# Performance work log

Measured on AMD Instinct MI355X. Metric: run time of the kernel, lower is better.

The kernel has to match this reference:

```python
import math
import jax, jax.numpy as jnp
import numpy as np

IN_CH = 512
KEY = 512
VAL = 512
B, T = 8, 2048
SQRT_KEY = math.sqrt(float(KEY))


def setup_inputs() -> dict:
    key = jax.random.key(0)
    ks = jax.random.split(key, 7)
    s_in = 1.0 / math.sqrt(IN_CH)
    return {
        "x": jax.random.normal(ks[0], (B, T, IN_CH), dtype=jnp.float32),
        "Wq": jax.random.uniform(ks[1], (IN_CH, KEY), jnp.float32, -s_in, s_in),
        "bq": jax.random.uniform(ks[2], (KEY,), jnp.float32, -s_in, s_in),
        "Wk": jax.random.uniform(ks[3], (IN_CH, KEY), jnp.float32, -s_in, s_in),
        "bk": jax.random.uniform(ks[4], (KEY,), jnp.float32, -s_in, s_in),
        "Wv": jax.random.uniform(ks[5], (IN_CH, VAL), jnp.float32, -s_in, s_in),
        "bv": jax.random.uniform(ks[6], (VAL,), jnp.float32, -s_in, s_in),
    }


def reference(x, Wq, bq, Wk, bk, Wv, bv):
    # x: [B, T, C]
    q = x @ Wq + bq          # [B, T, K]
    k = x @ Wk + bk          # [B, T, K]
    v = x @ Wv + bv          # [B, T, V]
    logits = jnp.einsum("btk,bsk->bts", q, k)  # [B, T(q), T(kv)]
    mask = jnp.tril(jnp.ones((T, T), dtype=bool))  # causal: key s <= query t
    logits = jnp.where(mask[None, :, :], logits, -jnp.inf)
    # NOTE: original torch code softmaxes over dim=1 (the QUERY axis) — kept faithful.
    probs = jax.nn.softmax(logits / SQRT_KEY, axis=1)
    read = jnp.einsum("bts,bsv->btv", probs, v)  # [B, T, V]
    return jnp.concatenate((x, read), axis=2)    # [B, T, C+V]
```

## Files before the change

### kernel.cpp

```cpp
#include <hip/hip_runtime.h>
#include <hip/hip_bf16.h>
#include <math.h>

#define BATCH 8
#define SEQ   2048
#define CH    512
#define ROWS  (BATCH * SEQ)
#define INVSQ 0.044194173824159216f

#define BM 128
#define BK 32
#define TILE_ELEMS (BM * BK)
#define TP 68

typedef __attribute__((ext_vector_type(8))) __bf16 bf16x8;
typedef __attribute__((ext_vector_type(4))) float f32x4;

__device__ inline unsigned short f2bf(float f) {
    unsigned u = __builtin_bit_cast(unsigned, f);
    u += 0x7fffu + ((u >> 16) & 1u);
    return (unsigned short)(u >> 16);
}
__device__ inline float bf2f(unsigned short s) {
    unsigned u = ((unsigned)s) << 16;
    return __builtin_bit_cast(float, u);
}

__device__ __forceinline__ void stage_tile(
    const unsigned short* __restrict__ gbase, size_t stride,
    unsigned short* lds, int wave, int lane)
{
#pragma unroll
    for (int j = 0; j < 2; ++j) {
        int chunk = wave * 2 + j;
        int row = chunk * 16 + (lane >> 2);
        const unsigned short* g = gbase + (size_t)row * stride + ((lane & 3) << 3);
        __builtin_amdgcn_global_load_lds(
            (const __attribute__((address_space(1))) unsigned int*)g,
            (__attribute__((address_space(3))) unsigned int*)(lds + (chunk << 9)),
            16, 0, 0);
    }
}

__device__ __forceinline__ void load_frags(
    const unsigned short* lds, int w0, int l16, int quad, bf16x8* f)
{
#pragma unroll
    for (int r = 0; r < 4; ++r)
        f[r] = *(const bf16x8*)(lds + (w0 + r * 16 + l16) * BK + quad * 8);
}

__global__ __launch_bounds__(256) void fuse_x_kernel(
    const float* __restrict__ x, unsigned short* __restrict__ xb,
    float* __restrict__ out, float* __restrict__ Z)
{
    if (blockIdx.x < 64) Z[blockIdx.x * 256 + threadIdx.x] = 0.f;
    size_t base = ((size_t)blockIdx.x * 256 + threadIdx.x) * 8;
    size_t row = base >> 9, c = base & 511;
    float4 v0 = *(const float4*)(x + base);
    float4 v1 = *(const float4*)(x + base + 4);
    float* o = out + row * 1024 + c;
    *(float4*)o = v0;
    *(float4*)(o + 4) = v1;
    alignas(16) unsigned short t[8];
    t[0] = f2bf(v0.x); t[1] = f2bf(v0.y); t[2] = f2bf(v0.z); t[3] = f2bf(v0.w);
    t[4] = f2bf(v1.x); t[5] = f2bf(v1.y); t[6] = f2bf(v1.z); t[7] = f2bf(v1.w);
    *(uint4*)(xb + base) = *(const uint4*)t;
}

__global__ __launch_bounds__(256) void transpose_w_kernel(
    const float* __restrict__ Wq, const float* __restrict__ Wk,
    const float* __restrict__ Wv, unsigned short* __restrict__ Wt)
{
    __shared__ unsigned short T[64 * TP];
    const int k0 = blockIdx.x * 64, n0 = blockIdx.y * 64, w = blockIdx.z;
    const float* W = (w == 0) ? Wq : (w == 1) ? Wk : Wv;
    const int tid = threadIdx.x;
#pragma unroll
    for (int i = 0; i < 2; ++i) {
        int slot = tid + i * 256;
        int kr = slot >> 3, c8 = (slot & 7) << 3;
        float4 a = *(const float4*)(W + (size_t)(k0 + kr) * CH + n0 + c8);
        float4 b = *(const float4*)(W + (size_t)(k0 + kr) * CH + n0 + c8 + 4);
        T[(c8 + 0) * TP + kr] = f2bf(a.x); T[(c8 + 1) * TP + kr] = f2bf(a.y);
        T[(c8 + 2) * TP + kr] = f2bf(a.z); T[(c8 + 3) * TP + kr] = f2bf(a.w);
        T[(c8 + 4) * TP + kr] = f2bf(b.x); T[(c8 + 5) * TP + kr] = f2bf(b.y);
        T[(c8 + 6) * TP + kr] = f2bf(b.z); T[(c8 + 7) * TP + kr] = f2bf(b.w);
    }
    __syncthreads();
#pragma unroll
    for (int i = 0; i < 2; ++i) {
        int slot = tid + i * 256;
        int nr = slot >> 3, k8 = (slot & 7) << 3;
        uint2 lo = *(const uint2*)(T + nr * TP + k8);
        uint2 hi = *(const uint2*)(T + nr * TP + k8 + 4);
        uint4 u; u.x = lo.x; u.y = lo.y; u.z = hi.x; u.w = hi.y;
        *(uint4*)(Wt + ((size_t)w * CH + n0 + nr) * CH + k0 + k8) = u;
    }
}

__global__ __launch_bounds__(256) void transpose_v_kernel(
    const unsigned short* __restrict__ vb, const float* __restrict__ Z,
    unsigned short* __restrict__ Vt)
{
    __shared__ unsigned short T[64 * TP];
    const int s0 = blockIdx.x * 64, v0 = blockIdx.y * 64, b = blockIdx.z;
    const int tid = threadIdx.x;
#pragma unroll
    for (int i = 0; i < 2; ++i) {
        int slot = tid + i * 256;
        int sr = slot >> 3, c8 = (slot & 7) << 3;
        float inv = 1.0f / Z[b * SEQ + s0 + sr];
        uint4 raw = *(const uint4*)(vb + ((size_t)b * SEQ + s0 + sr) * CH + v0 + c8);
        const unsigned short* p = (const unsigned short*)&raw;
#pragma unroll
        for (int j = 0; j < 8; ++j)
            T[(c8 + j) * TP + sr] = f2bf(bf2f(p[j]) * inv);
    }
    __syncthreads();
#pragma unroll
    for (int i = 0; i < 2; ++i) {
        int slot = tid + i * 256;
        int vr = slot >> 3, s8 = (slot & 7) << 3;
        uint2 lo = *(const uint2*)(T + vr * TP + s8);
        uint2 hi = *(const uint2*)(T + vr * TP + s8 + 4);
        uint4 u; u.x = lo.x; u.y = lo.y; u.z = hi.x; u.w = hi.y;
        *(uint4*)(Vt + ((size_t)b * CH + v0 + vr) * SEQ + s0 + s8) = u;
    }
}

#define MFMA_ROW(r, af) \
    acc[r][0] = __builtin_amdgcn_mfma_f32_16x16x32_bf16(af, b0, acc[r][0], 0, 0, 0); \
    acc[r][1] = __builtin_amdgcn_mfma_f32_16x16x32_bf16(af, b1, acc[r][1], 0, 0, 0); \
    acc[r][2] = __builtin_amdgcn_mfma_f32_16x16x32_bf16(af, b2, acc[r][2], 0, 0, 0); \
    acc[r][3] = __builtin_amdgcn_mfma_f32_16x16x32_bf16(af, b3, acc[r][3], 0, 0, 0);

#define PIPELINE_LOOP                                                         \
    stageA(0); stageB(0); stageB(1);                                          \
    asm volatile("s_waitcnt vmcnt(2)" ::: "memory");                          \
    __builtin_amdgcn_s_barrier();                                             \
    __builtin_amdgcn_sched_barrier(0);                                        \
    _Pragma("unroll")                                                         \
    for (int U = 0; U < 16; ++U) {                                            \
        const unsigned short* Ab = lds + (U & 1) * 4096;                      \
        const unsigned short* Bb = lds + 8192 + (U & 1) * 8192;               \
        bf16x8 a0, a1, b0, b1, b2, b3;                                        \
        b0 = *(const bf16x8*)(Bb + (brow +  0) * 32 + rswz);                  \
        b1 = *(const bf16x8*)(Bb + (brow + 16) * 32 + rswz);                  \
        b2 = *(const bf16x8*)(Bb + (brow + 32) * 32 + rswz);                  \
        b3 = *(const bf16x8*)(Bb + (brow + 48) * 32 + rswz);                  \
        a0 = *(const bf16x8*)(Ab + (arow +  0) * 32 + rswz);                  \
        a1 = *(const bf16x8*)(Ab + (arow + 16) * 32 + rswz);                  \
        stageA(U + 1);                                                        \
        __builtin_amdgcn_s_barrier();                                         \
        asm volatile("s_waitcnt lgkmcnt(0)" ::: "memory");                    \
        __builtin_amdgcn_sched_barrier(0);                                    \
        __builtin_amdgcn_s_setprio(1);                                        \
        MFMA_ROW(0, a0);                                                      \
        MFMA_ROW(1, a1);                                                      \
        __builtin_amdgcn_s_setprio(0);                                        \
        __builtin_amdgcn_s_barrier();                                         \
        __builtin_amdgcn_sched_barrier(0);                                    \
        a0 = *(const bf16x8*)(Ab + (arow + 32) * 32 + rswz);                  \
        a1 = *(const bf16x8*)(Ab + (arow + 48) * 32 + rswz);                  \
        stageB(U + 2);                                                        \
        __builtin_amdgcn_s_barrier();                                         \
        asm volatile("s_waitcnt lgkmcnt(0)" ::: "memory");                    \
        __builtin_amdgcn_sched_barrier(0);                                    \
        __builtin_amdgcn_s_setprio(1);                                        \
        MFMA_ROW(2, a0);                                                      \
        MFMA_ROW(3, a1);                                                      \
        __builtin_amdgcn_s_setprio(0);                                        \
        if (U <= 13)      asm volatile("s_waitcnt vmcnt(2)" ::: "memory");    \
        else if (U == 14) asm volatile("s_waitcnt vmcnt(0)" ::: "memory");    \
        __builtin_amdgcn_s_barrier();                                         \
        __builtin_amdgcn_sched_barrier(0);                                    \
    }

__global__ __launch_bounds__(512, 2) void qkv8_kernel(
    const unsigned short* __restrict__ xb, const unsigned short* __restrict__ Wt,
    const float* __restrict__ bq, const float* __restrict__ bk,
    const float* __restrict__ bv, unsigned short* __restrict__ qkv)
{
    __shared__ unsigned short lds[24576];
    const int tid = threadIdx.x;
    const int lane = tid & 63, wave = tid >> 6;
    const int waveA = wave >> 2;
    const int waveB = wave & 3;
    const int quad = lane >> 4, l16 = lane & 15;

    int id = (int)blockIdx.x;
    id = (id & 7) * 96 + (id >> 3);
    const int xt = id / 12, wt = id - xt * 12;
    const int xrow0 = xt << 8, wrow0 = wt << 7;

    const unsigned short* __restrict__ Wg = Wt + (size_t)wrow0 * CH;
    const unsigned short* __restrict__ Xg = xb + (size_t)xrow0 * CH;

    const int srow = tid >> 2;
    const int scol = (((tid & 3) ^ ((tid >> 3) & 3)) << 3);
    const size_t ga  = (size_t)srow * CH + scol;
    const size_t gb1 = (size_t)(srow + 128) * CH + scol;
    const int wdst = wave * 512;
    const int rswz = ((quad ^ ((l16 >> 1) & 3)) << 3);
    const int arow = waveA * 64 + l16;
    const int brow = waveB * 64 + l16;

    f32x4 acc[4][4] = {};

    auto stageA = [&](int V) {
        if (V >= 16) return;
        const unsigned short* g = Wg + ga + V * 32;
        unsigned short* d = lds + (V & 1) * 4096 + wdst;
        __builtin_amdgcn_global_load_lds(
            (const __attribute__((address_space(1))) unsigned int*)g,
            (__attribute__((address_space(3))) unsigned int*)d, 16, 0, 0);
    };
    auto stageB = [&](int V) {
        if (V >= 16) return;
        const unsigned short* g0 = Xg + ga + V * 32;
        const unsigned short* g1 = Xg + gb1 + V * 32;
        unsigned short* d = lds + 8192 + (V & 1) * 8192 + wdst;
        __builtin_amdgcn_global_load_lds(
            (const __attribute__((address_space(1))) unsigned int*)g0,
            (__attribute__((address_space(3))) unsigned int*)d, 16, 0, 0);
        __builtin_amdgcn_global_load_lds(
            (const __attribute__((address_space(1))) unsigned int*)g1,
            (__attribute__((address_space(3))) unsigned int*)(d + 4096), 16, 0, 0);
    };

    PIPELINE_LOOP

    const int which = wrow0 >> 9;
    const float* bias = (which == 0) ? bq : (which == 1) ? bk : bv;
    const float scale = (which == 0) ? INVSQ : 1.0f;
    unsigned short* outw = qkv + (size_t)which * ROWS * CH;
    const int colblk = wrow0 & 511;
#pragma unroll
    for (int r = 0; r < 4; ++r) {
        int colb = colblk + waveA * 64 + r * 16 + quad * 4;
        float4 b4 = *(const float4*)(bias + colb);
#pragma unroll
        for (int c = 0; c < 4; ++c) {
            int m = xrow0 + waveB * 64 + c * 16 + l16;
            alignas(8) unsigned short pk[4];
            pk[0] = f2bf((acc[r][c][0] + b4.x) * scale);
            pk[1] = f2bf((acc[r][c][1] + b4.y) * scale);
            pk[2] = f2bf((acc[r][c][2] + b4.z) * scale);
            pk[3] = f2bf((acc[r][c][3] + b4.w) * scale);
            *(uint2*)(outw + (size_t)m * CH + colb) = *(const uint2*)pk;
        }
    }
}

__global__ __launch_bounds__(512, 2) void logits8_kernel(
    const unsigned short* __restrict__ qb, const unsigned short* __restrict__ kb,
    unsigned short* __restrict__ E, float* __restrict__ Z)
{
    __shared__ unsigned short lds[24576];
    const int tid = threadIdx.x;
    const int lane = tid & 63, wave = tid >> 6;
    const int waveA = wave >> 2;
    const int waveB = wave & 3;
    const int quad = lane >> 4, l16 = lane & 15;

    const int b = (int)blockIdx.x & 7;
    const int i = (int)blockIdx.x >> 3;
    int tt2 = (int)((sqrtf(4.f * (float)i + 1.f) - 1.f) * 0.5f);
    int st = i - tt2 * (tt2 + 1);
    while (st < 0)           { --tt2; st = i - tt2 * (tt2 + 1); }
    while (st > 2 * tt2 + 1) { ++tt2; st = i - tt2 * (tt2 + 1); }
    const int m0s = st << 7;
    const int n0t = tt2 << 8;

    const unsigned short* __restrict__ Wg = kb + ((size_t)b * SEQ + m0s) * CH;
    const unsigned short* __restrict__ Xg = qb + ((size_t)b * SEQ + n0t) * CH;

    const int srow = tid >> 2;
    const int scol = (((tid & 3) ^ ((tid >> 3) & 3)) << 3);
    const size_t ga  = (size_t)srow * CH + scol;
    const size_t gb1 = (size_t)(srow + 128) * CH + scol;
    const int wdst = wave * 512;
    const int rswz = ((quad ^ ((l16 >> 1) & 3)) << 3);
    const int arow = waveA * 64 + l16;
    const int brow = waveB * 64 + l16;

    f32x4 acc[4][4] = {};

    auto stageA = [&](int V) {
        if (V >= 16) return;
        const unsigned short* g = Wg + ga + V * 32;
        unsigned short* d = lds + (V & 1) * 4096 + wdst;
        __builtin_amdgcn_global_load_lds(
            (const __attribute__((address_space(1))) unsigned int*)g,
            (__attribute__((address_space(3))) unsigned int*)d, 16, 0, 0);
    };
    auto stageB = [&](int V) {
        if (V >= 16) return;
        const unsigned short* g0 = Xg + ga + V * 32;
        const unsigned short* g1 = Xg + gb1 + V * 32;
        unsigned short* d = lds + 8192 + (V & 1) * 8192 + wdst;
        __builtin_amdgcn_global_load_lds(
            (const __attribute__((address_space(1))) unsigned int*)g0,
            (__attribute__((address_space(3))) unsigned int*)d, 16, 0, 0);
        __builtin_amdgcn_global_load_lds(
            (const __attribute__((address_space(1))) unsigned int*)g1,
            (__attribute__((address_space(3))) unsigned int*)(d + 4096), 16, 0, 0);
    };

    PIPELINE_LOOP

#pragma unroll
    for (int r = 0; r < 4; ++r) {
        int sb = m0s + waveA * 64 + r * 16 + quad * 4;
        float ev[4][4];
#pragma unroll
        for (int c = 0; c < 4; ++c) {
            int t = n0t + waveB * 64 + c * 16 + l16;
#pragma unroll
            for (int reg = 0; reg < 4; ++reg)
                ev[c][reg] = (sb + reg <= t) ? __expf(acc[r][c][reg]) : 0.f;
        }
#pragma unroll
        for (int reg = 0; reg < 4; ++reg) {
            float z = ev[0][reg] + ev[1][reg] + ev[2][reg] + ev[3][reg];
            z += __shfl_xor(z, 1);
            z += __shfl_xor(z, 2);
            z += __shfl_xor(z, 4);
            z += __shfl_xor(z, 8);
            if (l16 == 0) atomicAdd(&Z[b * SEQ + sb + reg], z);
        }
#pragma unroll
        for (int c = 0; c < 4; ++c) {
            int t = n0t + waveB * 64 + c * 16 + l16;
            alignas(8) unsigned short pk[4];
            pk[0] = f2bf(ev[c][0]); pk[1] = f2bf(ev[c][1]);
            pk[2] = f2bf(ev[c][2]); pk[3] = f2bf(ev[c][3]);
            *(uint2*)(E + ((size_t)b * SEQ + t) * SEQ + sb) = *(const uint2*)pk;
        }
    }
}
#undef PIPELINE_LOOP
#undef MFMA_ROW

__global__ __launch_bounds__(256) void read_kernel(
    const unsigned short* __restrict__ E, const unsigned short* __restrict__ Vt,
    float* __restrict__ out)
{
    __shared__ unsigned short As[2 * TILE_ELEMS];
    __shared__ unsigned short Bs[2 * TILE_ELEMS];
    const int id = blockIdx.x;
    const int b = id & 7;
    const int rem = id >> 3;
    const int mv = rem & 3;
    const int r0 = rem >> 2;
    const int tt = (r0 < 8) ? r0 : 23 - r0;
    const int m0v = mv * BM;
    const int n0t = tt * BM;
    const int Kmax = (tt + 1) * BM;
    const int tid = threadIdx.x;
    const int lane = tid & 63, wave = tid >> 6;
    const int wm = (wave >> 1) * 64, wn = (wave & 1) * 64;
    const int quad = lane >> 4, l16 = lane & 15;
    const unsigned short* Vb = Vt + (size_t)b * CH * SEQ;
    const unsigned short* Eb = E + (size_t)b * SEQ * SEQ;

    f32x4 acc[4][4] = {};
    for (int kk = 0; kk < Kmax; kk += 64) {
        stage_tile(Vb + (size_t)m0v * SEQ + kk,      SEQ, As,              wave, lane);
        stage_tile(Vb + (size_t)m0v * SEQ + kk + 32, SEQ, As + TILE_ELEMS, wave, lane);
        stage_tile(Eb + (size_t)n0t * SEQ + kk,      SEQ, Bs,              wave, lane);
        stage_tile(Eb + (size_t)n0t * SEQ + kk + 32, SEQ, Bs + TILE_ELEMS, wave, lane);
        __syncthreads();
#pragma unroll
        for (int h = 0; h < 2; ++h) {
            bf16x8 a[4], bb[4];
            load_frags(As + h * TILE_ELEMS, wm, l16, quad, a);
            load_frags(Bs + h * TILE_ELEMS, wn, l16, quad, bb);
#pragma unroll
            for (int r = 0; r < 4; ++r)
#pragma unroll
                for (int c = 0; c < 4; ++c)
                    acc[r][c] = __builtin_amdgcn_mfma_f32_16x16x32_bf16(a[r], bb[c], acc[r][c], 0, 0, 0);
        }
        __syncthreads();
    }
#pragma unroll
    for (int r = 0; r < 4; ++r) {
        int v = 512 + m0v + wm + r * 16 + quad * 4;
#pragma unroll
        for (int c = 0; c < 4; ++c) {
            int t = n0t + wn + c * 16 + l16;
            float4 f;
            f.x = acc[r][c][0]; f.y = acc[r][c][1];
            f.z = acc[r][c][2]; f.w = acc[r][c][3];
            *(float4*)(out + ((size_t)b * SEQ + t) * 1024 + v) = f;
        }
    }
}

extern "C" void kernel_launch(void* const* d_in, const int* in_sizes, int n_in,
                              void* d_out, int out_size, void* d_ws, size_t ws_size,
                              hipStream_t stream) {
    const float* x  = (const float*)d_in[0];
    const float* Wq = (const float*)d_in[1];
    const float* bq = (const float*)d_in[2];
    const float* Wk = (const float*)d_in[3];
    const float* bk = (const float*)d_in[4];
    const float* Wv = (const float*)d_in[5];
    const float* bv = (const float*)d_in[6];
    float* out = (float*)d_out;

    char* ws = (char*)d_ws;
    const size_t QKV_BYTES = (size_t)ROWS * CH * 2;
    const size_t E_BYTES   = (size_t)BATCH * SEQ * SEQ * 2;
    unsigned short* qkv = (unsigned short*)ws;
    unsigned short* qb = qkv;
    unsigned short* kb = (unsigned short*)(ws + QKV_BYTES);
    unsigned short* vb = (unsigned short*)(ws + 2 * QKV_BYTES);
    unsigned short* E  = (unsigned short*)(ws + 3 * QKV_BYTES);
    float* Z = (float*)(ws + 3 * QKV_BYTES + E_BYTES);
    unsigned short* xb = E;
    unsigned short* Wt = (unsigned short*)((char*)E + QKV_BYTES);
    unsigned short* Vt = qb;

    dim3 blk(256);
    fuse_x_kernel<<<dim3(4096), blk, 0, stream>>>(x, xb, out, Z);
    transpose_w_kernel<<<dim3(8, 8, 3), blk, 0, stream>>>(Wq, Wk, Wv, Wt);
    qkv8_kernel<<<dim3(768), dim3(512), 0, stream>>>(xb, Wt, bq, bk, bv, qkv);
    logits8_kernel<<<dim3(576), dim3(512), 0, stream>>>(qb, kb, E, Z);
    transpose_v_kernel<<<dim3(32, 8, 8), blk, 0, stream>>>(vb, Z, Vt);
    read_kernel<<<dim3(512), blk, 0, stream>>>(E, Vt, out);
}
```

Baseline: 234.8 us.

## Software-pipeline read kernel with double-buffered swizzled LDS and split MFMA phases

Replaces the simple load-sync-compute loop of the attention read GEMM with a double-buffered pipeline. Global-to-LDS loads for the next A and B tiles are issued while MFMAs run on the current tile, with explicit vmcnt/lgkmcnt waits and barriers. An XOR swizzle on the LDS layout aims to cut bank conflicts, and setprio favours the MFMA waves. Launch bounds now request two blocks per CU. The risk is subtle waitcnt or barrier ordering bugs and a larger instruction count per iteration.

```diff
diff --git a/kernel.cpp b/kernel.cpp
--- a/kernel.cpp
+++ b/kernel.cpp
@@ -9,8 +9,6 @@
 #define INVSQ 0.044194173824159216f
 
 #define BM 128
-#define BK 32
-#define TILE_ELEMS (BM * BK)
 #define TP 68
 
 typedef __attribute__((ext_vector_type(8))) __bf16 bf16x8;
@@ -24,30 +22,6 @@
 __device__ inline float bf2f(unsigned short s) {
     unsigned u = ((unsigned)s) << 16;
     return __builtin_bit_cast(float, u);
-}
-
-__device__ __forceinline__ void stage_tile(
-    const unsigned short* __restrict__ gbase, size_t stride,
-    unsigned short* lds, int wave, int lane)
-{
-#pragma unroll
-    for (int j = 0; j < 2; ++j) {
-        int chunk = wave * 2 + j;
-        int row = chunk * 16 + (lane >> 2);
-        const unsigned short* g = gbase + (size_t)row * stride + ((lane & 3) << 3);
-        __builtin_amdgcn_global_load_lds(
-            (const __attribute__((address_space(1))) unsigned int*)g,
-            (__attribute__((address_space(3))) unsigned int*)(lds + (chunk << 9)),
-            16, 0, 0);
-    }
-}
-
-__device__ __forceinline__ void load_frags(
-    const unsigned short* lds, int w0, int l16, int quad, bf16x8* f)
-{
-#pragma unroll
-    for (int r = 0; r < 4; ++r)
-        f[r] = *(const bf16x8*)(lds + (w0 + r * 16 + l16) * BK + quad * 8);
 }
 
 __global__ __launch_bounds__(256) void fuse_x_kernel(
@@ -341,14 +315,18 @@
     }
 }
 #undef PIPELINE_LOOP
-#undef MFMA_ROW
-
-__global__ __launch_bounds__(256) void read_kernel(
+
+__global__ __launch_bounds__(256, 2) void read8_kernel(
     const unsigned short* __restrict__ E, const unsigned short* __restrict__ Vt,
     float* __restrict__ out)
 {
-    __shared__ unsigned short As[2 * TILE_ELEMS];
-    __shared__ unsigned short Bs[2 * TILE_ELEMS];
+    __shared__ unsigned short lds[16384];
+    const int tid = threadIdx.x;
+    const int lane = tid & 63, wave = tid >> 6;
+    const int waveA = wave >> 1;
+    const int waveB = wave & 1;
+    const int quad = lane >> 4, l16 = lane & 15;
+
     const int id = blockIdx.x;
     const int b = id & 7;
     const int rem = id >> 3;
@@ -357,40 +335,95 @@
     const int tt = (r0 < 8) ? r0 : 23 - r0;
     const int m0v = mv * BM;
     const int n0t = tt * BM;
-    const int Kmax = (tt + 1) * BM;
-    const int tid = threadIdx.x;
-    const int lane = tid & 63, wave = tid >> 6;
-    const int wm = (wave >> 1) * 64, wn = (wave & 1) * 64;
-    const int quad = lane >> 4, l16 = lane & 15;
-    const unsigned short* Vb = Vt + (size_t)b * CH * SEQ;
-    const unsigned short* Eb = E + (size_t)b * SEQ * SEQ;
+    const int NT = (tt + 1) * 4;
+
+    const unsigned short* __restrict__ Ag = Vt + ((size_t)b * CH + m0v) * SEQ;
+    const unsigned short* __restrict__ Bg = E + ((size_t)b * SEQ + n0t) * SEQ;
+
+    const int scol = (((lane & 3) ^ ((lane >> 3) & 3)) << 3);
+    const int srow = wave * 16 + (lane >> 2);
+    const size_t ga0 = (size_t)srow * SEQ + scol;
+    const size_t ga1 = (size_t)(srow + 64) * SEQ + scol;
+    const int wdst = wave * 512;
+    const int rswz = ((quad ^ ((l16 >> 1) & 3)) << 3);
+    const int arow = waveA * 64 + l16;
+    const int brow = waveB * 64 + l16;
 
     f32x4 acc[4][4] = {};
-    for (int kk = 0; kk < Kmax; kk += 64) {
-        stage_tile(Vb + (size_t)m0v * SEQ + kk,      SEQ, As,              wave, lane);
-        stage_tile(Vb + (size_t)m0v * SEQ + kk + 32, SEQ, As + TILE_ELEMS, wave, lane);
-        stage_tile(Eb + (size_t)n0t * SEQ + kk,      SEQ, Bs,              wave, lane);
-        stage_tile(Eb + (size_t)n0t * SEQ + kk + 32, SEQ, Bs + TILE_ELEMS, wave, lane);
-        __syncthreads();
-#pragma unroll
-        for (int h = 0; h < 2; ++h) {
-            bf16x8 a[4], bb[4];
-            load_frags(As + h * TILE_ELEMS, wm, l16, quad, a);
-            load_frags(Bs + h * TILE_ELEMS, wn, l16, quad, bb);
-#pragma unroll
-            for (int r = 0; r < 4; ++r)
-#pragma unroll
-                for (int c = 0; c < 4; ++c)
-                    acc[r][c] = __builtin_amdgcn_mfma_f32_16x16x32_bf16(a[r], bb[c], acc[r][c], 0, 0, 0);
-        }
-        __syncthreads();
-    }
+
+    auto stageA = [&](int V) {
+        if (V >= NT) return;
+        const unsigned short* g0 = Ag + ga0 + V * 32;
+        const unsigned short* g1 = Ag + ga1 + V * 32;
+        unsigned short* d = lds + (V & 1) * 4096 + wdst;
+        __builtin_amdgcn_global_load_lds(
+            (const __attribute__((address_space(1))) unsigned int*)g0,
+            (__attribute__((address_space(3))) unsigned int*)d, 16, 0, 0);
+        __builtin_amdgcn_global_load_lds(
+            (const __attribute__((address_space(1))) unsigned int*)g1,
+            (__attribute__((address_space(3))) unsigned int*)(d + 2048), 16, 0, 0);
+    };
+    auto stageB = [&](int V) {
+        if (V >= NT) return;
+        const unsigned short* g0 = Bg + ga0 + V * 32;
+        const unsigned short* g1 = Bg + ga1 + V * 32;
+        unsigned short* d = lds + 8192 + (V & 1) * 4096 + wdst;
+        __builtin_amdgcn_global_load_lds(
+            (const __attribute__((address_space(1))) unsigned int*)g0,
+            (__attribute__((address_space(3))) unsigned int*)d, 16, 0, 0);
+        __builtin_amdgcn_global_load_lds(
+            (const __attribute__((address_space(1))) unsigned int*)g1,
+            (__attribute__((address_space(3))) unsigned int*)(d + 2048), 16, 0, 0);
+    };
+
+    stageA(0); stageB(0); stageB(1);
+    asm volatile("s_waitcnt vmcnt(2)" ::: "memory");
+    __builtin_amdgcn_s_barrier();
+    __builtin_amdgcn_sched_barrier(0);
+
+#pragma unroll 2
+    for (int U = 0; U < NT; ++U) {
+        const unsigned short* Ab = lds + (U & 1) * 4096;
+        const unsigned short* Bb = lds + 8192 + (U & 1) * 4096;
+        bf16x8 a0, a1, b0, b1, b2, b3;
+        b0 = *(const bf16x8*)(Bb + (brow +  0) * 32 + rswz);
+        b1 = *(const bf16x8*)(Bb + (brow + 16) * 32 + rswz);
+        b2 = *(const bf16x8*)(Bb + (brow + 32) * 32 + rswz);
+        b3 = *(const bf16x8*)(Bb + (brow + 48) * 32 + rswz);
+        a0 = *(const bf16x8*)(Ab + (arow +  0) * 32 + rswz);
+        a1 = *(const bf16x8*)(Ab + (arow + 16) * 32 + rswz);
+        stageA(U + 1);
+        __builtin_amdgcn_s_barrier();
+        asm volatile("s_waitcnt lgkmcnt(0)" ::: "memory");
+        __builtin_amdgcn_sched_barrier(0);
+        __builtin_amdgcn_s_setprio(1);
+        MFMA_ROW(0, a0);
+        MFMA_ROW(1, a1);
+        __builtin_amdgcn_s_setprio(0);
+        __builtin_amdgcn_s_barrier();
+        __builtin_amdgcn_sched_barrier(0);
+        a0 = *(const bf16x8*)(Ab + (arow + 32) * 32 + rswz);
+        a1 = *(const bf16x8*)(Ab + (arow + 48) * 32 + rswz);
+        stageB(U + 2);
+        __builtin_amdgcn_s_barrier();
+        asm volatile("s_waitcnt lgkmcnt(0)" ::: "memory");
+        __builtin_amdgcn_sched_barrier(0);
+        __builtin_amdgcn_s_setprio(1);
+        MFMA_ROW(2, a0);
+        MFMA_ROW(3, a1);
+        __builtin_amdgcn_s_setprio(0);
+        if (U <= NT - 3)      asm volatile("s_waitcnt vmcnt(2)" ::: "memory");
+        else if (U == NT - 2) asm volatile("s_waitcnt vmcnt(0)" ::: "memory");
+        __builtin_amdgcn_s_barrier();
+        __builtin_amdgcn_sched_barrier(0);
+    }
+
 #pragma unroll
     for (int r = 0; r < 4; ++r) {
-        int v = 512 + m0v + wm + r * 16 + quad * 4;
+        int v = 512 + m0v + waveA * 64 + r * 16 + quad * 4;
 #pragma unroll
         for (int c = 0; c < 4; ++c) {
-            int t = n0t + wn + c * 16 + l16;
+            int t = n0t + waveB * 64 + c * 16 + l16;
             float4 f;
             f.x = acc[r][c][0]; f.y = acc[r][c][1];
             f.z = acc[r][c][2]; f.w = acc[r][c][3];
@@ -398,6 +431,7 @@
         }
     }
 }
+#undef MFMA_ROW
 
 extern "C" void kernel_launch(void* const* d_in, const int* in_sizes, int n_in,
                               void* d_out, int out_size, void* d_ws, size_t ws_size,
@@ -430,5 +464,5 @@
     qkv8_kernel<<<dim3(768), dim3(512), 0, stream>>>(xb, Wt, bq, bk, bv, qkv);
     logits8_kernel<<<dim3(576), dim3(512), 0, stream>>>(qb, kb, E, Z);
     transpose_v_kernel<<<dim3(32, 8, 8), blk, 0, stream>>>(vb, Z, Vt);
-    read_kernel<<<dim3(512), blk, 0, stream>>>(E, Vt, out);
-}
+    read8_kernel<<<dim3(512), blk, 0, stream>>>(E, Vt, out);
+}
```

Measured after the change: 224.7 us. 4.3% less time.
